# Performance work log

Hardware: AMD Instinct MI355X
Metric: run time of the kernel (lower is better)

Reference implementation:

```python
import jax, jax.numpy as jnp
import numpy as np

B, S, H, L, NH, V = 8, 512, 768, 12, 12, 21128
DH = H // NH
FF = 4 * H
PAD_ID, SEP_ID = 0, 102
EPS = 1e-12


def _ln(x, g, b):
    mu = jnp.mean(x, axis=-1, keepdims=True)
    var = jnp.mean(jnp.square(x - mu), axis=-1, keepdims=True)
    return (x - mu) * jax.lax.rsqrt(var + EPS) * g + b


def setup_inputs() -> dict:
    key = jax.random.key(0)
    ks = jax.random.split(key, 24)
    # token ids with a per-sample [SEP] boundary and trailing padding
    ids = jax.random.randint(ks[0], (B, S), 1, V)
    qpos = jax.random.randint(ks[1], (B,), 16, 64)
    seqlen = jax.random.randint(ks[2], (B,), 384, S + 1)
    pos = jnp.arange(S)
    ids = jnp.where(pos[None, :] == qpos[:, None], SEP_ID, ids)
    ids = jnp.where(pos[None, :] < seqlen[:, None], ids, PAD_ID)

    w = lambda k, shape: (jax.random.normal(k, shape, dtype=jnp.float32) * 0.02)
    return {
        "input_ids": ids,
        "word_emb": w(ks[3], (V, H)),
        "pos_emb": w(ks[4], (S, H)),
        "type_emb": w(ks[5], (2, H)),
        "emb_ln_g": jnp.ones((H,), jnp.float32),
        "emb_ln_b": jnp.zeros((H,), jnp.float32),
        "attn_w": w(ks[6], (L, 4, H, H)),     # q,k,v,o projections
        "attn_b": w(ks[7], (L, 4, H)),
        "ln1_g": jnp.ones((L, H), jnp.float32),
        "ln1_b": jnp.zeros((L, H), jnp.float32),
        "ffn_w1": w(ks[8], (L, H, FF)),
        "ffn_b1": w(ks[9], (L, FF)),
        "ffn_w2": w(ks[10], (L, FF, H)),
        "ffn_b2": w(ks[11], (L, H)),
        "ln2_g": jnp.ones((L, H), jnp.float32),
        "ln2_b": jnp.zeros((L, H), jnp.float32),
        "cls_w": w(ks[12], (H, V)),
        "cls_b": jnp.zeros((V,), jnp.float32),
    }


def _qa_causal_bias(input_ids):
    # Faithful to make_qa_causal_mask: pad mask * (bidirectional over question,
    # causal over answer), boundary = first [SEP] position + 1 per sample.
    pad = input_ids != PAD_ID                                  # [B,S]
    qlen = jnp.argmax(input_ids == SEP_ID, axis=1) + 1          # [B]
    i = jnp.arange(S)[:, None]
    j = jnp.arange(S)[None, :]
    in_answer = (i[None] >= qlen[:, None, None]) & (j[None] >= qlen[:, None, None])
    causal_ok = jnp.where(in_answer, j <= i, True)              # [B,S,S]
    mask = pad[:, :, None] & pad[:, None, :] & causal_ok
    return jnp.where(mask, 0.0, -1e9).astype(jnp.float32)       # additive bias


def reference(input_ids, word_emb, pos_emb, type_emb, emb_ln_g, emb_ln_b,
              attn_w, attn_b, ln1_g, ln1_b, ffn_w1, ffn_b1, ffn_w2, ffn_b2,
              ln2_g, ln2_b, cls_w, cls_b):
    bias = _qa_causal_bias(input_ids)[:, None]                  # [B,1,S,S]
    h = word_emb[input_ids] + pos_emb[None, :S] + type_emb[0]
    h = _ln(h, emb_ln_g, emb_ln_b)
    scale = 1.0 / jnp.sqrt(jnp.float32(DH))
    for l in range(L):
        wq, wk, wv, wo = attn_w[l]
        bq, bk, bv, bo = attn_b[l]
        q = (h @ wq + bq).reshape(B, S, NH, DH)
        k = (h @ wk + bk).reshape(B, S, NH, DH)
        v = (h @ wv + bv).reshape(B, S, NH, DH)
        scores = jnp.einsum('bqhd,bkhd->bhqk', q, k) * scale + bias
        probs = jax.nn.softmax(scores, axis=-1)
        ctx = jnp.einsum('bhqk,bkhd->bqhd', probs, v).reshape(B, S, H)
        h = _ln(h + ctx @ wo + bo, ln1_g[l], ln1_b[l])
        ff = jax.nn.gelu(h @ ffn_w1[l] + ffn_b1[l], approximate=False) @ ffn_w2[l] + ffn_b2[l]
        h = _ln(h + ff, ln2_g[l], ln2_b[l])
    return h @ cls_w + cls_b                                    # [B,S,V] logits
```

## Files before the change

kernel.cpp:

```cpp
#include <hip/hip_runtime.h>
#include <hip/hip_bf16.h>
#include <stdint.h>

#define BB   8
#define SS   512
#define HH   768
#define LL   12
#define NHH  12
#define DHH  64
#define FFF  3072
#define VV   21128
#define PAD_ID 0
#define SEP_ID 102
#define BS   (BB*SS)
#define BSH  ((size_t)BS*HH)
#define BSFF ((size_t)BS*FFF)
#define QKVN (3*HH)

using bf16 = __hip_bfloat16;
typedef __attribute__((ext_vector_type(8))) short short8;
typedef __attribute__((ext_vector_type(4))) short short4v;
typedef __attribute__((ext_vector_type(4))) float f32x4;

__device__ __forceinline__ f32x4 Z4() { f32x4 z = {0.f, 0.f, 0.f, 0.f}; return z; }

__device__ __forceinline__ void gload16(void* lds, const void* g) {
    __builtin_amdgcn_global_load_lds(
        (const __attribute__((address_space(1))) uint32_t*)g,
        (__attribute__((address_space(3))) uint32_t*)(uint32_t)(uintptr_t)lds,
        16, 0, 0);
}

template <int N>
__device__ __forceinline__ void waitvm() {
    if constexpr (N == 0) asm volatile("s_waitcnt vmcnt(0)" ::: "memory");
    else if constexpr (N == 2) asm volatile("s_waitcnt vmcnt(2)" ::: "memory");
    else if constexpr (N == 3) asm volatile("s_waitcnt vmcnt(3)" ::: "memory");
    else if constexpr (N == 4) asm volatile("s_waitcnt vmcnt(4)" ::: "memory");
    else if constexpr (N == 6) asm volatile("s_waitcnt vmcnt(6)" ::: "memory");
    else asm volatile("s_waitcnt vmcnt(8)" ::: "memory");
    __builtin_amdgcn_sched_barrier(0);
}

__device__ __forceinline__ void barrier_raw() {
    __builtin_amdgcn_s_barrier();
    __builtin_amdgcn_sched_barrier(0);
}

__device__ __forceinline__ void wait_vm0_lgkm0_barrier() {
    asm volatile("s_waitcnt vmcnt(0) lgkmcnt(0)" ::: "memory");
    __builtin_amdgcn_sched_barrier(0);
    __builtin_amdgcn_s_barrier();
    __builtin_amdgcn_sched_barrier(0);
}

__global__ void __launch_bounds__(256) qlen_kernel(const int* __restrict__ ids,
                                                   int* __restrict__ qlen) {
    int b = blockIdx.x, tid = threadIdx.x;
    __shared__ int red[256];
    int best = 1 << 30;
    for (int j = tid; j < SS; j += 256)
        if (ids[b * SS + j] == SEP_ID) best = min(best, j);
    red[tid] = best; __syncthreads();
    for (int off = 128; off > 0; off >>= 1) {
        if (tid < off) red[tid] = min(red[tid], red[tid + off]);
        __syncthreads();
    }
    if (tid == 0) qlen[b] = (red[0] == (1 << 30) ? 0 : red[0]) + 1;
}

__device__ __forceinline__ float block_reduce_sum(float v, float* red, int tid) {
    red[tid] = v; __syncthreads();
    for (int off = 128; off > 0; off >>= 1) {
        if (tid < off) red[tid] += red[tid + off];
        __syncthreads();
    }
    float r = red[0]; __syncthreads();
    return r;
}

__global__ void __launch_bounds__(256) embed_ln_kernel(
    const int* __restrict__ ids, const float* __restrict__ we,
    const float* __restrict__ pe, const float* __restrict__ te,
    const float* __restrict__ g, const float* __restrict__ bt,
    float* __restrict__ h, bf16* __restrict__ hb) {
    int token = blockIdx.x, tid = threadIdx.x;
    int s = token % SS;
    int id = ids[token];
    __shared__ float red[256];
    float x[3];
#pragma unroll
    for (int i = 0; i < 3; ++i) {
        int idx = tid + i * 256;
        x[i] = we[(size_t)id * HH + idx] + pe[(size_t)s * HH + idx] + te[idx];
    }
    float sum = block_reduce_sum(x[0] + x[1] + x[2], red, tid);
    float mu = sum * (1.0f / HH);
    float vs = 0.f;
#pragma unroll
    for (int i = 0; i < 3; ++i) { float d = x[i] - mu; vs += d * d; }
    vs = block_reduce_sum(vs, red, tid);
    float rstd = rsqrtf(vs * (1.0f / HH) + 1e-12f);
    size_t base = (size_t)token * HH;
#pragma unroll
    for (int i = 0; i < 3; ++i) {
        int idx = tid + i * 256;
        float v = (x[i] - mu) * rstd * g[idx] + bt[idx];
        h[base + idx] = v;
        hb[base + idx] = __float2bfloat16(v);
    }
}

__global__ void __launch_bounds__(256) add_ln_kernel(
    float* __restrict__ h, const float* __restrict__ proj,
    const float* __restrict__ proj2,
    const float* __restrict__ g, const float* __restrict__ bt,
    bf16* __restrict__ hb) {
    int token = blockIdx.x, tid = threadIdx.x;
    __shared__ float red[256];
    size_t base = (size_t)token * HH;
    float x[3];
#pragma unroll
    for (int i = 0; i < 3; ++i) {
        int idx = tid + i * 256;
        x[i] = h[base + idx] + proj[base + idx] + proj2[base + idx];
    }
    float sum = block_reduce_sum(x[0] + x[1] + x[2], red, tid);
    float mu = sum * (1.0f / HH);
    float vs = 0.f;
#pragma unroll
    for (int i = 0; i < 3; ++i) { float d = x[i] - mu; vs += d * d; }
    vs = block_reduce_sum(vs, red, tid);
    float rstd = rsqrtf(vs * (1.0f / HH) + 1e-12f);
#pragma unroll
    for (int i = 0; i < 3; ++i) {
        int idx = tid + i * 256;
        float v = (x[i] - mu) * rstd * g[idx] + bt[idx];
        h[base + idx] = v;
        hb[base + idx] = __float2bfloat16(v);
    }
}

__global__ void __launch_bounds__(256) transp_conv(
    const float* __restrict__ in, bf16* __restrict__ out,
    int K, int N, size_t inStride, size_t outStride) {
    const float* src = in + (size_t)blockIdx.z * inStride;
    bf16* dst = out + (size_t)blockIdx.z * outStride;
    __shared__ float t[64][65];
    int n0 = blockIdx.x * 64, k0 = blockIdx.y * 64;
    int tid = threadIdx.x;
    int r = tid >> 4, c4 = (tid & 15) * 4;
#pragma unroll
    for (int i = 0; i < 4; ++i) {
        int kk = k0 + r + i * 16;
        int n = n0 + c4;
        float4 v;
        if (n + 3 < N) {
            v = *(const float4*)(src + (size_t)kk * N + n);
        } else {
            v.x = (n + 0 < N) ? src[(size_t)kk * N + n + 0] : 0.f;
            v.y = (n + 1 < N) ? src[(size_t)kk * N + n + 1] : 0.f;
            v.z = (n + 2 < N) ? src[(size_t)kk * N + n + 2] : 0.f;
            v.w = (n + 3 < N) ? src[(size_t)kk * N + n + 3] : 0.f;
        }
        t[c4 + 0][r + i * 16] = v.x;
        t[c4 + 1][r + i * 16] = v.y;
        t[c4 + 2][r + i * 16] = v.z;
        t[c4 + 3][r + i * 16] = v.w;
    }
    __syncthreads();
#pragma unroll
    for (int i = 0; i < 4; ++i) {
        int nn = n0 + r + i * 16;
        if (nn < N) {
            short4v o;
            o[0] = (short)__bfloat16_as_ushort(__float2bfloat16(t[r + i * 16][c4 + 0]));
            o[1] = (short)__bfloat16_as_ushort(__float2bfloat16(t[r + i * 16][c4 + 1]));
            o[2] = (short)__bfloat16_as_ushort(__float2bfloat16(t[r + i * 16][c4 + 2]));
            o[3] = (short)__bfloat16_as_ushort(__float2bfloat16(t[r + i * 16][c4 + 3]));
            *(short4v*)(dst + (size_t)nn * K + k0 + c4) = o;
        }
    }
}

__global__ void __launch_bounds__(256) vtrans_kernel(const bf16* __restrict__ v,
                                                     bf16* __restrict__ vT,
                                                     int ldv) {
    __shared__ bf16 t[64][68];
    int s0 = blockIdx.x * 64, h = blockIdx.y, b = blockIdx.z;
    int tid = threadIdx.x;
    int r = tid >> 4, c4 = (tid & 15) * 4;
#pragma unroll
    for (int i = 0; i < 4; ++i) {
        int sr = r + i * 16;
        short4v x = *(const short4v*)(v + ((size_t)(b * SS + s0 + sr)) * ldv +
                                      h * 64 + c4);
        t[c4 + 0][sr] = __ushort_as_bfloat16((unsigned short)x[0]);
        t[c4 + 1][sr] = __ushort_as_bfloat16((unsigned short)x[1]);
        t[c4 + 2][sr] = __ushort_as_bfloat16((unsigned short)x[2]);
        t[c4 + 3][sr] = __ushort_as_bfloat16((unsigned short)x[3]);
    }
    __syncthreads();
#pragma unroll
    for (int i = 0; i < 4; ++i) {
        int dr = r + i * 16;
        short4v o;
        o[0] = (short)__bfloat16_as_ushort(t[dr][c4 + 0]);
        o[1] = (short)__bfloat16_as_ushort(t[dr][c4 + 1]);
        o[2] = (short)__bfloat16_as_ushort(t[dr][c4 + 2]);
        o[3] = (short)__bfloat16_as_ushort(t[dr][c4 + 3]);
        *(short4v*)(vT + (((size_t)(b * NHH + h)) * 64 + dr) * SS + s0 + c4) = o;
    }
}

#define GBK 32

template <int TBM, int TBN, int OUT_BF16, int ACT, int KK, int LDA, int LDB,
          int LDC, int NN, int NSTAGES>
__global__ void __launch_bounds__(256) gemm_bf16_kernel(
    const bf16* __restrict__ A, const bf16* __restrict__ BT,
    const float* __restrict__ bias, void* __restrict__ Cout, size_t zStride) {
    constexpr int MFRAG = TBM / 32;
    constexpr int NFRAG = TBN / 32;
    constexpr int ABYTES = TBM * GBK * 2;
    constexpr int BBYTES = TBN * GBK * 2;
    constexpr int LPS = TBM / 64 + TBN / 64;
    __shared__ __align__(16) char As[NSTAGES * ABYTES];
    __shared__ __align__(16) char Bs[NSTAGES * BBYTES];
    int tid = threadIdx.x;
    int lane = tid & 63, wid = tid >> 6;

    int zz = blockIdx.z;
    const char* Ab = (const char*)(A + (size_t)zz * KK);
    const char* Bb = (const char*)(BT + (size_t)zz * KK);

    int gN = gridDim.x, gM = gridDim.y;
    int nwg = gN * gM;
    int bid = blockIdx.y * gN + blockIdx.x;
    int swz = ((nwg & 7) == 0) ? ((bid & 7) * (nwg >> 3) + (bid >> 3)) : bid;
    int width = 8 * gN;
    int grp = swz / width, rem = swz % width;
    int gh = min(8, gM - grp * 8);
    int by = grp * 8 + rem % gh;
    int bx = rem / gh;

    int m0 = by * TBM, n0 = bx * TBN;
    int wr = (wid >> 1) * (TBM / 2), wc = (wid & 1) * (TBN / 2);

    f32x4 acc[MFRAG][NFRAG];
#pragma unroll
    for (int i = 0; i < MFRAG; ++i)
#pragma unroll
        for (int j = 0; j < NFRAG; ++j) acc[i][j] = Z4();

    auto stage = [&](int k0, int sel) {
#pragma unroll
        for (int i = 0; i < TBM / 64; ++i) {
            int lin = tid * 16 + i * 4096;
            int row = lin >> 6, slot = (lin >> 4) & 3;
            gload16(As + sel * ABYTES + lin,
                    Ab + ((size_t)(m0 + row) * LDA + k0) * 2 +
                        ((slot ^ ((row >> 1) & 3)) << 4));
        }
#pragma unroll
        for (int i = 0; i < TBN / 64; ++i) {
            int lin = tid * 16 + i * 4096;
            int row = lin >> 6, slot = (lin >> 4) & 3;
            int nr = n0 + row;
            if constexpr (NN % TBN != 0) { if (nr >= NN) nr = NN - 1; }
            gload16(Bs + sel * BBYTES + lin,
                    Bb + ((size_t)nr * LDB + k0) * 2 +
                        ((slot ^ ((row >> 1) & 3)) << 4));
        }
    };

    constexpr int T = KK / GBK;
#pragma unroll
    for (int s = 0; s < NSTAGES - 1; ++s) stage(s * GBK, s);
    waitvm<(NSTAGES - 2) * LPS>();
    barrier_raw();

    for (int t = 0; t < T; ++t) {
        if (t + NSTAGES - 1 < T)
            stage((t + NSTAGES - 1) * GBK, (t + NSTAGES - 1) % NSTAGES);

        const char* Ar = As + (t % NSTAGES) * ABYTES;
        const char* Br = Bs + (t % NSTAGES) * BBYTES;
        short8 af[MFRAG], bfr[NFRAG];
#pragma unroll
        for (int i = 0; i < MFRAG; ++i) {
            int ar = wr + i * 16 + (lane & 15);
            int slot = (lane >> 4) ^ ((ar >> 1) & 3);
            af[i] = *(const short8*)(Ar + ar * 64 + slot * 16);
        }
#pragma unroll
        for (int j = 0; j < NFRAG; ++j) {
            int br = wc + j * 16 + (lane & 15);
            int slot = (lane >> 4) ^ ((br >> 1) & 3);
            bfr[j] = *(const short8*)(Br + br * 64 + slot * 16);
        }
#pragma unroll
        for (int i = 0; i < MFRAG; ++i)
#pragma unroll
            for (int j = 0; j < NFRAG; ++j)
                acc[i][j] = __builtin_amdgcn_mfma_f32_16x16x32_bf16(
                    af[i], bfr[j], acc[i][j], 0, 0, 0);

        if (t + 1 < T) {
            if constexpr (NSTAGES == 4) {
                if (t + 3 < T)      waitvm<2 * LPS>();
                else if (t + 2 < T) waitvm<LPS>();
                else                waitvm<0>();
            } else {
                if (t + 2 < T)      waitvm<LPS>();
                else                waitvm<0>();
            }
            barrier_raw();
        }
    }

    bool nfull = (NN % TBN == 0) || (n0 + TBN <= NN);
#pragma unroll
    for (int i = 0; i < MFRAG; ++i) {
#pragma unroll
        for (int r = 0; r < 4; ++r) {
            int m = m0 + wr + i * 16 + (lane >> 4) * 4 + r;
#pragma unroll
            for (int j = 0; j < NFRAG; ++j) {
                int n = n0 + wc + j * 16 + (lane & 15);
                if (nfull || n < NN) {
                    float v = acc[i][j][r] + ((zz == 0) ? bias[n] : 0.f);
                    if (ACT) v = 0.5f * v * (1.0f + erff(v * 0.70710678118654752f));
                    if (OUT_BF16)
                        ((bf16*)Cout)[(size_t)m * LDC + n] = __float2bfloat16(v);
                    else
                        ((float*)Cout)[zz * zStride + (size_t)m * LDC + n] = v;
                }
            }
        }
    }
}

__global__ void __launch_bounds__(256) attn_mfma_kernel(
    const bf16* __restrict__ Q, const bf16* __restrict__ K,
    const bf16* __restrict__ VT, const int* __restrict__ ids,
    const int* __restrict__ qlen, bf16* __restrict__ att, int ld) {
    __shared__ __align__(16) bf16 Qs[64 * 64];
    __shared__ __align__(16) bf16 Ks[2][64 * 64];
    __shared__ __align__(16) bf16 Vs[2][64 * 64];
    __shared__ __align__(16) bf16 Ps[4 * 16 * 64];
    __shared__ float padj[2][64];

    int tid = threadIdx.x, lane = tid & 63, w = tid >> 6;
    int q0 = blockIdx.x * 64, h = blockIdx.y, b = blockIdx.z;
    int ql = qlen[b];

    const char* kbase0 = (const char*)K + ((size_t)(b * SS) * ld) * 2;
    const char* vbase0 = (const char*)VT + (((size_t)(b * NHH + h)) * 64) * SS * 2;

    auto stageKV = [&](int kv0, int sel) {
        int lin = tid * 16;
#pragma unroll
        for (int i = 0; i < 2; ++i, lin += 4096) {
            int row = lin >> 7, bir = lin & 127;
            int sbir = bir ^ ((row & 7) << 4);
            gload16((char*)Ks[sel] + lin,
                    kbase0 + (size_t)(kv0 + row) * (ld * 2) + h * 128 + sbir);
            gload16((char*)Vs[sel] + lin,
                    vbase0 + (size_t)row * (SS * 2) + (size_t)kv0 * 2 + sbir);
        }
        if (tid < 64)
            padj[sel][tid] = (ids[b * SS + kv0 + tid] != PAD_ID) ? 1.f : 0.f;
    };

    {
        const char* qbase =
            (const char*)Q + ((size_t)(b * SS + q0) * ld) * 2 + h * 128;
        int lin = tid * 16;
#pragma unroll
        for (int i = 0; i < 2; ++i, lin += 4096) {
            int row = lin >> 7, bir = lin & 127;
            int sbir = bir ^ ((row & 7) << 4);
            gload16((char*)Qs + lin, qbase + (size_t)row * (ld * 2) + sbir);
        }
    }
    stageKV(0, 0);
    int qrow_base = q0 + w * 16 + (lane >> 4) * 4;
    bool padq[4];
#pragma unroll
    for (int r = 0; r < 4; ++r)
        padq[r] = (ids[b * SS + qrow_base + r] != PAD_ID);

    wait_vm0_lgkm0_barrier();

    short8 aq[2];
#pragma unroll
    for (int ks = 0; ks < 2; ++ks) {
        int row = w * 16 + (lane & 15);
        int bir = ks * 64 + (lane >> 4) * 16;
        aq[ks] = *(const short8*)((const char*)Qs + row * 128 +
                                  (bir ^ ((row & 7) << 4)));
    }

    float m_run[4], l_run[4];
    f32x4 accO[4];
#pragma unroll
    for (int r = 0; r < 4; ++r) { m_run[r] = -1e30f; l_run[r] = 0.f; }
#pragma unroll
    for (int d = 0; d < 4; ++d) accO[d] = Z4();

    int cur = 0;
    for (int kv0 = 0; kv0 < SS; kv0 += 64) {
        if (kv0 + 64 < SS) stageKV(kv0 + 64, cur ^ 1);
        const char* kb = (const char*)Ks[cur];
        const char* vb = (const char*)Vs[cur];

        f32x4 accS[4];
        __builtin_amdgcn_s_setprio(1);
#pragma unroll
        for (int nf = 0; nf < 4; ++nf) {
            f32x4 z = Z4();
#pragma unroll
            for (int ks = 0; ks < 2; ++ks) {
                int row = nf * 16 + (lane & 15);
                int bir = ks * 64 + (lane >> 4) * 16;
                short8 bk = *(const short8*)(kb + row * 128 +
                                             (bir ^ ((row & 7) << 4)));
                z = __builtin_amdgcn_mfma_f32_16x16x32_bf16(aq[ks], bk, z, 0, 0, 0);
            }
            accS[nf] = z;
        }
        __builtin_amdgcn_s_setprio(0);

        float p[4][4];
#pragma unroll
        for (int r = 0; r < 4; ++r) {
            int qg = qrow_base + r;
            float mx = -1e30f;
#pragma unroll
            for (int nf = 0; nf < 4; ++nf) {
                int j = kv0 + nf * 16 + (lane & 15);
                bool ok = padq[r] && (padj[cur][nf * 16 + (lane & 15)] != 0.f) &&
                          ((qg < ql) || (j < ql) || (j <= qg));
                float s = accS[nf][r] * 0.125f + (ok ? 0.f : -1e9f);
                p[r][nf] = s;
                mx = fmaxf(mx, s);
            }
#pragma unroll
            for (int off = 1; off < 16; off <<= 1)
                mx = fmaxf(mx, __shfl_xor(mx, off));
            float mnew = fmaxf(m_run[r], mx);
            float fac = __expf(m_run[r] - mnew);
            m_run[r] = mnew;
            float rs = 0.f;
#pragma unroll
            for (int nf = 0; nf < 4; ++nf) {
                float e = __expf(p[r][nf] - mnew);
                p[r][nf] = e;
                rs += e;
            }
#pragma unroll
            for (int off = 1; off < 16; off <<= 1)
                rs += __shfl_xor(rs, off);
            l_run[r] = l_run[r] * fac + rs;
#pragma unroll
            for (int df = 0; df < 4; ++df) accO[df][r] *= fac;
        }

#pragma unroll
        for (int r = 0; r < 4; ++r) {
            int prow = (lane >> 4) * 4 + r;
#pragma unroll
            for (int nf = 0; nf < 4; ++nf) {
                int c = nf * 16 + (lane & 15);
                int byte = (c * 2) ^ ((prow & 7) << 4);
                *(bf16*)((char*)Ps + w * 2048 + prow * 128 + byte) =
                    __float2bfloat16(p[r][nf]);
            }
        }
        asm volatile("s_waitcnt lgkmcnt(0)" ::: "memory");
        __builtin_amdgcn_sched_barrier(0);

        __builtin_amdgcn_s_setprio(1);
#pragma unroll
        for (int ks = 0; ks < 2; ++ks) {
            int prow = lane & 15;
            int bir = ks * 64 + (lane >> 4) * 16;
            short8 ap = *(const short8*)((const char*)Ps + w * 2048 + prow * 128 +
                                         (bir ^ ((prow & 7) << 4)));
#pragma unroll
            for (int df = 0; df < 4; ++df) {
                int vrow = df * 16 + (lane & 15);
                short8 bv = *(const short8*)(vb + vrow * 128 +
                                             (bir ^ ((vrow & 7) << 4)));
                accO[df] = __builtin_amdgcn_mfma_f32_16x16x32_bf16(
                    ap, bv, accO[df], 0, 0, 0);
            }
        }
        __builtin_amdgcn_s_setprio(0);

        if (kv0 + 64 < SS) wait_vm0_lgkm0_barrier();
        cur ^= 1;
    }

#pragma unroll
    for (int r = 0; r < 4; ++r) {
        int qg = qrow_base + r;
        float inv = 1.0f / l_run[r];
#pragma unroll
        for (int df = 0; df < 4; ++df) {
            int d = df * 16 + (lane & 15);
            att[((size_t)(b * SS) + qg) * HH + h * 64 + d] =
                __float2bfloat16(accO[df][r] * inv);
        }
    }
}

extern "C" void kernel_launch(void* const* d_in, const int* in_sizes, int n_in,
                              void* d_out, int out_size, void* d_ws, size_t ws_size,
                              hipStream_t stream) {
    const int*   ids      = (const int*)d_in[0];
    const float* word_emb = (const float*)d_in[1];
    const float* pos_emb  = (const float*)d_in[2];
    const float* type_emb = (const float*)d_in[3];
    const float* emb_ln_g = (const float*)d_in[4];
    const float* emb_ln_b = (const float*)d_in[5];
    const float* attn_w   = (const float*)d_in[6];
    const float* attn_b   = (const float*)d_in[7];
    const float* ln1_g    = (const float*)d_in[8];
    const float* ln1_b    = (const float*)d_in[9];
    const float* ffn_w1   = (const float*)d_in[10];
    const float* ffn_b1   = (const float*)d_in[11];
    const float* ffn_w2   = (const float*)d_in[12];
    const float* ffn_b2   = (const float*)d_in[13];
    const float* ln2_g    = (const float*)d_in[14];
    const float* ln2_b    = (const float*)d_in[15];
    const float* cls_w    = (const float*)d_in[16];
    const float* cls_b    = (const float*)d_in[17];
    float* out = (float*)d_out;

    char* base = (char*)d_ws;
    size_t off = 0;
    auto take = [&](size_t bytes) {
        char* r = base + off;
        off += (bytes + 255) & ~(size_t)255;
        return r;
    };
    float* h    = (float*)take(BSH * 4);
    float* proj = (float*)take(2 * BSH * 4);
    bf16*  qkv  = (bf16*)take((size_t)BS * QKVN * 2);
    bf16*  vT   = (bf16*)take(BSH * 2);
    bf16*  attb = (bf16*)take(BSH * 2);
    bf16*  ffb  = (bf16*)take(BSFF * 2);
    bf16*  hb   = (bf16*)take(BSH * 2);
    int*   qlen = (int*)take(256);
    size_t commonEnd = off;

    const size_t szAttnW = (size_t)48 * HH * HH * 2;
    const size_t szW1    = (size_t)LL * HH * FFF * 2;
    const size_t szCls   = (size_t)VV * HH * 2;
    const size_t fullNeed = commonEnd + szAttnW + 2 * szW1 + szCls;
    bool fullMode = (ws_size >= fullNeed);

    bf16 *wAttnT = nullptr, *w1T = nullptr, *w2T = nullptr, *clsT = nullptr, *wrot = nullptr;
    if (fullMode) {
        wAttnT = (bf16*)take(szAttnW);
        w1T    = (bf16*)take(szW1);
        w2T    = (bf16*)take(szW1);
        clsT   = (bf16*)take(szCls);
    } else {
        wrot = (bf16*)take((size_t)HH * FFF * 2);
        clsT = (bf16*)proj;
    }

    auto convw = [&](const float* src, bf16* dst, int K, int N) {
        dim3 g((N + 63) / 64, K / 64, 1);
        transp_conv<<<g, 256, 0, stream>>>(src, dst, K, N, (size_t)0, (size_t)0);
    };

    qlen_kernel<<<BB, 256, 0, stream>>>(ids, qlen);

    if (fullMode) {
        transp_conv<<<dim3(12, 12, 48), 256, 0, stream>>>(
            attn_w, wAttnT, HH, HH, (size_t)HH * HH, (size_t)HH * HH);
        transp_conv<<<dim3(FFF / 64, HH / 64, LL), 256, 0, stream>>>(
            ffn_w1, w1T, HH, FFF, (size_t)HH * FFF, (size_t)HH * FFF);
        transp_conv<<<dim3(HH / 64, FFF / 64, LL), 256, 0, stream>>>(
            ffn_w2, w2T, FFF, HH, (size_t)HH * FFF, (size_t)HH * FFF);
        transp_conv<<<dim3((VV + 63) / 64, HH / 64, 1), 256, 0, stream>>>(
            cls_w, clsT, HH, VV, (size_t)0, (size_t)0);
    }

    embed_ln_kernel<<<BS, 256, 0, stream>>>(ids, word_emb, pos_emb, type_emb,
                                            emb_ln_g, emb_ln_b, h, hb);

    dim3 gQKV(QKVN / 128, BS / 128, 1);
    dim3 gWo(HH / 64, BS / 128, 2);
    dim3 gFF1(FFF / 128, BS / 128, 1);
    dim3 gFF2(HH / 64, BS / 128, 2);
    dim3 gCls((VV + 127) / 128, BS / 128, 1);
    dim3 gAttn(SS / 64, NHH, BB);
    dim3 gVT(SS / 64, NHH, BB);

    for (int l = 0; l < LL; ++l) {
        const float* wq32 = attn_w + (size_t)l * 4 * HH * HH;
        const float* wo32 = wq32 + (size_t)3 * HH * HH;
        const float* bqkv = attn_b + (size_t)l * 4 * HH;
        const float* bo   = bqkv + 3 * HH;

        bf16 *wqkvT, *woT, *w1Tl, *w2Tl;
        if (fullMode) {
            wqkvT = wAttnT + (size_t)(l * 4) * HH * HH;
            woT   = wAttnT + (size_t)(l * 4 + 3) * HH * HH;
            w1Tl  = w1T + (size_t)l * HH * FFF;
            w2Tl  = w2T + (size_t)l * HH * FFF;
        } else {
            wqkvT = woT = w1Tl = w2Tl = wrot;
        }

        if (!fullMode) {
            convw(wq32, wrot, HH, HH);
            convw(wq32 + (size_t)HH * HH, wrot + (size_t)HH * HH, HH, HH);
            convw(wq32 + (size_t)2 * HH * HH, wrot + (size_t)2 * HH * HH, HH, HH);
        }
        gemm_bf16_kernel<128, 128, 1, 0, HH, HH, HH, QKVN, QKVN, 3>
            <<<gQKV, 256, 0, stream>>>(hb, wqkvT, bqkv, qkv, 0);

        vtrans_kernel<<<gVT, 256, 0, stream>>>(qkv + 2 * HH, vT, QKVN);
        attn_mfma_kernel<<<gAttn, 256, 0, stream>>>(
            qkv, qkv + HH, vT, ids, qlen, attb, QKVN);

        if (!fullMode) convw(wo32, wrot, HH, HH);
        gemm_bf16_kernel<128, 64, 0, 0, HH / 2, HH, HH, HH, HH, 3>
            <<<gWo, 256, 0, stream>>>(attb, woT, bo, proj, BSH);
        add_ln_kernel<<<BS, 256, 0, stream>>>(h, proj, proj + BSH,
                                              ln1_g + (size_t)l * HH,
                                              ln1_b + (size_t)l * HH, hb);

        if (!fullMode) convw(ffn_w1 + (size_t)l * HH * FFF, wrot, HH, FFF);
        gemm_bf16_kernel<128, 128, 1, 1, HH, HH, HH, FFF, FFF, 3>
            <<<gFF1, 256, 0, stream>>>(hb, w1Tl, ffn_b1 + (size_t)l * FFF, ffb, 0);
        if (!fullMode) convw(ffn_w2 + (size_t)l * HH * FFF, wrot, FFF, HH);
        gemm_bf16_kernel<128, 64, 0, 0, FFF / 2, FFF, FFF, HH, HH, 3>
            <<<gFF2, 256, 0, stream>>>(ffb, w2Tl, ffn_b2 + (size_t)l * HH, proj,
                                       BSH);
        add_ln_kernel<<<BS, 256, 0, stream>>>(h, proj, proj + BSH,
                                              ln2_g + (size_t)l * HH,
                                              ln2_b + (size_t)l * HH, hb);
    }

    if (!fullMode) convw(cls_w, clsT, HH, VV);
    gemm_bf16_kernel<128, 128, 0, 0, HH, HH, HH, VV, VV, 4>
        <<<gCls, 256, 0, stream>>>(hb, clsT, cls_b, out, 0);
}
```

Before: 2.807 ms.

## Use 512-thread blocks with 2x4 wave grid for 128x128 GEMMs

Templates the GEMM kernel on thread count. The 128x128 tiles (QKV, FFN1, classifier) now launch 512 threads arranged as 2x4 waves, so each wave holds fewer accumulator fragments and more waves are available to hide latency. Load issue counts and the wait counts are derived from the thread count. The classifier GEMM also drops from 4 to 3 pipeline stages, and the 4-stage wait logic is removed. The trade-off is less register reuse per wave and more LDS fragment reads per MFMA.

```diff
diff --git a/kernel.cpp b/kernel.cpp
--- a/kernel.cpp
+++ b/kernel.cpp
@@ -215,18 +215,23 @@
 
 #define GBK 32
 
-template <int TBM, int TBN, int OUT_BF16, int ACT, int KK, int LDA, int LDB,
-          int LDC, int NN, int NSTAGES>
-__global__ void __launch_bounds__(256) gemm_bf16_kernel(
+template <int THREADS, int TBM, int TBN, int OUT_BF16, int ACT, int KK,
+          int LDA, int LDB, int LDC, int NN, int NSTAGES>
+__global__ void __launch_bounds__(THREADS) gemm_bf16_kernel(
     const bf16* __restrict__ A, const bf16* __restrict__ BT,
     const float* __restrict__ bias, void* __restrict__ Cout, size_t zStride) {
-    constexpr int MFRAG = TBM / 32;
-    constexpr int NFRAG = TBN / 32;
+    constexpr int WN = (THREADS == 512) ? 4 : 2;
+    constexpr int WM = 2;
+    constexpr int MFRAG = TBM / WM / 16;
+    constexpr int NFRAG = TBN / WN / 16;
     constexpr int ABYTES = TBM * GBK * 2;
     constexpr int BBYTES = TBN * GBK * 2;
-    constexpr int LPS = TBM / 64 + TBN / 64;
-    __shared__ __align__(16) char As[NSTAGES * ABYTES];
-    __shared__ __align__(16) char Bs[NSTAGES * BBYTES];
+    constexpr int A_ISS = ABYTES / (THREADS * 16);
+    constexpr int B_ISS = BBYTES / (THREADS * 16);
+    constexpr int LPS = A_ISS + B_ISS;
+    __shared__ __align__(16) char smem[NSTAGES * (ABYTES + BBYTES)];
+    char* Asm = smem;
+    char* Bsm = smem + NSTAGES * ABYTES;
     int tid = threadIdx.x;
     int lane = tid & 63, wid = tid >> 6;
 
@@ -245,7 +250,8 @@
     int bx = rem / gh;
 
     int m0 = by * TBM, n0 = bx * TBN;
-    int wr = (wid >> 1) * (TBM / 2), wc = (wid & 1) * (TBN / 2);
+    int wr = (wid / WN) * (TBM / WM);
+    int wc = (wid % WN) * (TBN / WN);
 
     f32x4 acc[MFRAG][NFRAG];
 #pragma unroll
@@ -255,20 +261,20 @@
 
     auto stage = [&](int k0, int sel) {
 #pragma unroll
-        for (int i = 0; i < TBM / 64; ++i) {
-            int lin = tid * 16 + i * 4096;
+        for (int i = 0; i < A_ISS; ++i) {
+            int lin = tid * 16 + i * (THREADS * 16);
             int row = lin >> 6, slot = (lin >> 4) & 3;
-            gload16(As + sel * ABYTES + lin,
+            gload16(Asm + sel * ABYTES + lin,
                     Ab + ((size_t)(m0 + row) * LDA + k0) * 2 +
                         ((slot ^ ((row >> 1) & 3)) << 4));
         }
 #pragma unroll
-        for (int i = 0; i < TBN / 64; ++i) {
-            int lin = tid * 16 + i * 4096;
+        for (int i = 0; i < B_ISS; ++i) {
+            int lin = tid * 16 + i * (THREADS * 16);
             int row = lin >> 6, slot = (lin >> 4) & 3;
             int nr = n0 + row;
             if constexpr (NN % TBN != 0) { if (nr >= NN) nr = NN - 1; }
-            gload16(Bs + sel * BBYTES + lin,
+            gload16(Bsm + sel * BBYTES + lin,
                     Bb + ((size_t)nr * LDB + k0) * 2 +
                         ((slot ^ ((row >> 1) & 3)) << 4));
         }
@@ -284,8 +290,8 @@
         if (t + NSTAGES - 1 < T)
             stage((t + NSTAGES - 1) * GBK, (t + NSTAGES - 1) % NSTAGES);
 
-        const char* Ar = As + (t % NSTAGES) * ABYTES;
-        const char* Br = Bs + (t % NSTAGES) * BBYTES;
+        const char* Ar = Asm + (t % NSTAGES) * ABYTES;
+        const char* Br = Bsm + (t % NSTAGES) * BBYTES;
         short8 af[MFRAG], bfr[NFRAG];
 #pragma unroll
         for (int i = 0; i < MFRAG; ++i) {
@@ -307,14 +313,8 @@
                     af[i], bfr[j], acc[i][j], 0, 0, 0);
 
         if (t + 1 < T) {
-            if constexpr (NSTAGES == 4) {
-                if (t + 3 < T)      waitvm<2 * LPS>();
-                else if (t + 2 < T) waitvm<LPS>();
-                else                waitvm<0>();
-            } else {
-                if (t + 2 < T)      waitvm<LPS>();
-                else                waitvm<0>();
-            }
+            if (t + 2 < T) waitvm<LPS>();
+            else           waitvm<0>();
             barrier_raw();
         }
     }
@@ -623,25 +623,25 @@
             convw(wq32 + (size_t)HH * HH, wrot + (size_t)HH * HH, HH, HH);
             convw(wq32 + (size_t)2 * HH * HH, wrot + (size_t)2 * HH * HH, HH, HH);
         }
-        gemm_bf16_kernel<128, 128, 1, 0, HH, HH, HH, QKVN, QKVN, 3>
-            <<<gQKV, 256, 0, stream>>>(hb, wqkvT, bqkv, qkv, 0);
+        gemm_bf16_kernel<512, 128, 128, 1, 0, HH, HH, HH, QKVN, QKVN, 3>
+            <<<gQKV, 512, 0, stream>>>(hb, wqkvT, bqkv, qkv, 0);
 
         vtrans_kernel<<<gVT, 256, 0, stream>>>(qkv + 2 * HH, vT, QKVN);
         attn_mfma_kernel<<<gAttn, 256, 0, stream>>>(
             qkv, qkv + HH, vT, ids, qlen, attb, QKVN);
 
         if (!fullMode) convw(wo32, wrot, HH, HH);
-        gemm_bf16_kernel<128, 64, 0, 0, HH / 2, HH, HH, HH, HH, 3>
+        gemm_bf16_kernel<256, 128, 64, 0, 0, HH / 2, HH, HH, HH, HH, 3>
             <<<gWo, 256, 0, stream>>>(attb, woT, bo, proj, BSH);
         add_ln_kernel<<<BS, 256, 0, stream>>>(h, proj, proj + BSH,
                                               ln1_g + (size_t)l * HH,
                                               ln1_b + (size_t)l * HH, hb);
 
         if (!fullMode) convw(ffn_w1 + (size_t)l * HH * FFF, wrot, HH, FFF);
-        gemm_bf16_kernel<128, 128, 1, 1, HH, HH, HH, FFF, FFF, 3>
-            <<<gFF1, 256, 0, stream>>>(hb, w1Tl, ffn_b1 + (size_t)l * FFF, ffb, 0);
+        gemm_bf16_kernel<512, 128, 128, 1, 1, HH, HH, HH, FFF, FFF, 3>
+            <<<gFF1, 512, 0, stream>>>(hb, w1Tl, ffn_b1 + (size_t)l * FFF, ffb, 0);
         if (!fullMode) convw(ffn_w2 + (size_t)l * HH * FFF, wrot, FFF, HH);
-        gemm_bf16_kernel<128, 64, 0, 0, FFF / 2, FFF, FFF, HH, HH, 3>
+        gemm_bf16_kernel<256, 128, 64, 0, 0, FFF / 2, FFF, FFF, HH, HH, 3>
             <<<gFF2, 256, 0, stream>>>(ffb, w2Tl, ffn_b2 + (size_t)l * HH, proj,
                                        BSH);
         add_ln_kernel<<<BS, 256, 0, stream>>>(h, proj, proj + BSH,
@@ -650,6 +650,6 @@
     }
 
     if (!fullMode) convw(cls_w, clsT, HH, VV);
-    gemm_bf16_kernel<128, 128, 0, 0, HH, HH, HH, VV, VV, 4>
-        <<<gCls, 256, 0, stream>>>(hb, clsT, cls_b, out, 0);
-}
+    gemm_bf16_kernel<512, 128, 128, 0, 0, HH, HH, HH, VV, VV, 3>
+        <<<gCls, 512, 0, stream>>>(hb, clsT, cls_b, out, 0);
+}
```

Result: faster. 2.638 ms (-6.0%).
